# Kernel tuning notes

Measured on AMD Instinct MI355X. Metric: run time of the kernel, lower is better.

The kernel has to match this reference:

```python
import jax, jax.numpy as jnp
import numpy as np

B = 65536
IN2 = 256      # input_shape * 2
H2 = 512       # rnn_hidden_dim * 2
A = 32         # n_actions


def setup_inputs() -> dict:
    key = jax.random.key(0)
    ks = jax.random.split(key, 12)
    s = lambda k, shape, fan: jax.random.normal(k, shape, jnp.float32) / np.sqrt(fan)
    return {
        "inputs": jax.random.normal(ks[0], (B, IN2), jnp.float32),
        "hidden_state": jax.random.normal(ks[1], (B, H2), jnp.float32),
        "W1": s(ks[2], (H2, IN2), IN2),
        "b1": jnp.zeros((H2,), jnp.float32),
        "W_ih": s(ks[3], (3 * H2, H2), H2),
        "W_hh": s(ks[4], (3 * H2, H2), H2),
        "b_ih": jnp.zeros((3 * H2,), jnp.float32),
        "b_hh": jnp.zeros((3 * H2,), jnp.float32),
        "W21": s(ks[5], (A, H2), H2),
        "b21": jnp.zeros((A,), jnp.float32),
        "W22": s(ks[6], (A, H2), H2),
        "b22": jnp.zeros((A,), jnp.float32),
    }


def _forward(inputs, hidden_state, W1, b1, W_ih, W_hh, b_ih, b_hh, W21, b21, W22, b22):
    # fc1 + ReLU
    x = jax.nn.relu(inputs @ W1.T + b1)                      # [B, H2]
    h_in = hidden_state.reshape(-1, H2)
    # PyTorch GRUCell semantics
    gi = x @ W_ih.T + b_ih                                   # [B, 3*H2]
    gh = h_in @ W_hh.T + b_hh                                # [B, 3*H2]
    i_r, i_z, i_n = jnp.split(gi, 3, axis=1)
    h_r, h_z, h_n = jnp.split(gh, 3, axis=1)
    r = jax.nn.sigmoid(i_r + h_r)
    z = jax.nn.sigmoid(i_z + h_z)
    n = jnp.tanh(i_n + r * h_n)
    h = (1.0 - z) * n + z * h_in                             # [B, H2]
    # two Q heads
    q1 = h @ W21.T + b21                                     # [B, A]
    q2 = h @ W22.T + b22                                     # [B, A]
    # vectorized row-interleave (replaces the nested Python loop)
    q = jnp.stack([q1, q2], axis=1).reshape(2 * q1.shape[0], q1.shape[1])  # [2B, A]
    return q, h


def reference(inputs, hidden_state, W1, b1, W_ih, W_hh, b_ih, b_hh, W21, b21, W22, b22):
    return _forward(inputs, hidden_state, W1, b1, W_ih, W_hh, b_ih, b_hh, W21, b21, W22, b22)
```

## Files before the change

### kernel.cpp

```cpp
#include <hip/hip_runtime.h>


#define BATCH 65536
#define IN2   256
#define H2    512
#define NA    32
#define QELEMS (2 * BATCH * NA)

typedef float  f32x4  __attribute__((ext_vector_type(4)));
typedef short  short8 __attribute__((ext_vector_type(8)));
typedef __bf16 bf16x8 __attribute__((ext_vector_type(8)));

__device__ __forceinline__ f32x4 mfma16(short8 a, short8 b, f32x4 c) {
  return __builtin_amdgcn_mfma_f32_16x16x32_bf16(
      __builtin_bit_cast(bf16x8, a), __builtin_bit_cast(bf16x8, b), c, 0, 0, 0);
}

__device__ __forceinline__ unsigned short f2bf(float f) {
  union { float f; unsigned u; } v; v.f = f;
  unsigned r = v.u + 0x7fffu + ((v.u >> 16) & 1u);
  return (unsigned short)(r >> 16);
}

__global__ void cvt_kernel(const float* __restrict__ s,
                           unsigned short* __restrict__ d, int n4) {
  for (int i = blockIdx.x * blockDim.x + threadIdx.x; i < n4;
       i += gridDim.x * blockDim.x) {
    float4 f = ((const float4*)s)[i];
    ushort4 o;
    o.x = f2bf(f.x); o.y = f2bf(f.y); o.z = f2bf(f.z); o.w = f2bf(f.w);
    ((ushort4*)d)[i] = o;
  }
}

__global__ __launch_bounds__(256, 2)
void fc1_kernel(const unsigned short* __restrict__ A,
                const unsigned short* __restrict__ W,
                const float* __restrict__ bias,
                unsigned short* __restrict__ X) {
  __shared__ unsigned short As[128][72];
  __shared__ unsigned short Bs[64][72];
  const int tid  = threadIdx.x;
  const int lane = tid & 63, wid = tid >> 6;
  const int l16 = lane & 15, kg = (lane >> 4) * 8, rbase = (lane >> 4) * 4;
  const int row0 = blockIdx.x * 128;
  const int col0 = blockIdx.y * 64;
  const int wrow = (wid >> 1) * 64;
  const int wcol = (wid & 1) * 32;

  f32x4 acc[4][2] = {};

  for (int k0 = 0; k0 < IN2; k0 += 64) {
#pragma unroll
    for (int c = 0; c < 4; ++c) {
      int idx = tid + c * 256;
      int r = idx >> 3, k8 = idx & 7;
      uint4 v = *(const uint4*)&A[(row0 + r) * IN2 + k0 + k8 * 8];
      *(uint4*)&As[r][k8 * 8] = v;
    }
#pragma unroll
    for (int c = 0; c < 2; ++c) {
      int idx = tid + c * 256;
      int r = idx >> 3, k8 = idx & 7;
      uint4 v = *(const uint4*)&W[(col0 + r) * IN2 + k0 + k8 * 8];
      *(uint4*)&Bs[r][k8 * 8] = v;
    }
    __syncthreads();
#pragma unroll
    for (int kk = 0; kk < 64; kk += 32) {
      short8 af[4], bf[2];
#pragma unroll
      for (int m = 0; m < 4; ++m)
        af[m] = *(const short8*)&As[wrow + m * 16 + l16][kk + kg];
#pragma unroll
      for (int n = 0; n < 2; ++n)
        bf[n] = *(const short8*)&Bs[wcol + n * 16 + l16][kk + kg];
#pragma unroll
      for (int m = 0; m < 4; ++m)
#pragma unroll
        for (int n = 0; n < 2; ++n)
          acc[m][n] = mfma16(af[m], bf[n], acc[m][n]);
    }
    __syncthreads();
  }

#pragma unroll
  for (int m = 0; m < 4; ++m)
#pragma unroll
    for (int n = 0; n < 2; ++n) {
      int col = col0 + wcol + n * 16 + l16;
      float bv = bias[col];
#pragma unroll
      for (int e = 0; e < 4; ++e) {
        int row = row0 + wrow + m * 16 + rbase + e;
        float v = acc[m][n][e] + bv;
        v = v > 0.f ? v : 0.f;
        X[row * H2 + col] = f2bf(v);
      }
    }
}

__global__ __launch_bounds__(256, 2)
void gru_kernel(const unsigned short* __restrict__ X16,
                const unsigned short* __restrict__ H16,
                const unsigned short* __restrict__ Wih,
                const unsigned short* __restrict__ Whh,
                const float* __restrict__ b_ih,
                const float* __restrict__ b_hh,
                const float* __restrict__ hidden,
                float* __restrict__ out_h) {
  __shared__ unsigned short Xs[128][72];
  __shared__ unsigned short Hs[128][72];
  __shared__ unsigned short Ws[6][32][72];

  const int tid  = threadIdx.x;
  const int lane = tid & 63, wid = tid >> 6;
  const int l16 = lane & 15, kg = (lane >> 4) * 8, rbase = (lane >> 4) * 4;
  const int row0 = blockIdx.x * 128;
  const int j0   = blockIdx.y * 32;
  const int wrow = wid * 32;

  f32x4 accI[3][2][2] = {};
  f32x4 accH[3][2][2] = {};

  for (int k0 = 0; k0 < H2; k0 += 64) {
#pragma unroll
    for (int c = 0; c < 4; ++c) {
      int idx = tid + c * 256;
      int r = idx >> 3, k8 = idx & 7;
      *(uint4*)&Xs[r][k8 * 8] =
          *(const uint4*)&X16[(row0 + r) * H2 + k0 + k8 * 8];
    }
#pragma unroll
    for (int c = 0; c < 4; ++c) {
      int idx = tid + c * 256;
      int r = idx >> 3, k8 = idx & 7;
      *(uint4*)&Hs[r][k8 * 8] =
          *(const uint4*)&H16[(row0 + r) * H2 + k0 + k8 * 8];
    }
#pragma unroll
    for (int c = 0; c < 6; ++c) {
      int idx = tid + c * 256;
      int slab = idx >> 8, rem = idx & 255;
      int r = rem >> 3, k8 = rem & 7;
      const unsigned short* src =
          (slab < 3) ? &Wih[(slab * H2 + j0 + r) * H2]
                     : &Whh[((slab - 3) * H2 + j0 + r) * H2];
      *(uint4*)&Ws[slab][r][k8 * 8] = *(const uint4*)&src[k0 + k8 * 8];
    }
    __syncthreads();
#pragma unroll
    for (int kk = 0; kk < 64; kk += 32) {
      short8 ax[2], ah[2], bw[6][2];
#pragma unroll
      for (int m = 0; m < 2; ++m) {
        ax[m] = *(const short8*)&Xs[wrow + m * 16 + l16][kk + kg];
        ah[m] = *(const short8*)&Hs[wrow + m * 16 + l16][kk + kg];
      }
#pragma unroll
      for (int g = 0; g < 6; ++g)
#pragma unroll
        for (int n = 0; n < 2; ++n)
          bw[g][n] = *(const short8*)&Ws[g][n * 16 + l16][kk + kg];
#pragma unroll
      for (int g = 0; g < 3; ++g)
#pragma unroll
        for (int m = 0; m < 2; ++m)
#pragma unroll
          for (int n = 0; n < 2; ++n) {
            accI[g][m][n] = mfma16(ax[m], bw[g][n], accI[g][m][n]);
            accH[g][m][n] = mfma16(ah[m], bw[3 + g][n], accH[g][m][n]);
          }
    }
    __syncthreads();
  }

#pragma unroll
  for (int m = 0; m < 2; ++m)
#pragma unroll
    for (int n = 0; n < 2; ++n) {
      int j = j0 + n * 16 + l16;
      float bir = b_ih[j],        bhr = b_hh[j];
      float biz = b_ih[H2 + j],   bhz = b_hh[H2 + j];
      float bin = b_ih[2*H2 + j], bhn = b_hh[2*H2 + j];
#pragma unroll
      for (int e = 0; e < 4; ++e) {
        int row = row0 + wrow + m * 16 + rbase + e;
        float ir = accI[0][m][n][e] + bir;
        float iz = accI[1][m][n][e] + biz;
        float in_ = accI[2][m][n][e] + bin;
        float hr = accH[0][m][n][e] + bhr;
        float hz = accH[1][m][n][e] + bhz;
        float hn = accH[2][m][n][e] + bhn;
        float r = 1.f / (1.f + __expf(-(ir + hr)));
        float z = 1.f / (1.f + __expf(-(iz + hz)));
        float nn = tanhf(in_ + r * hn);
        float hp = hidden[row * H2 + j];
        out_h[row * H2 + j] = (1.f - z) * nn + z * hp;
      }
    }
}

__global__ __launch_bounds__(256, 2)
void heads_kernel(const float* __restrict__ Hsrc,
                  const unsigned short* __restrict__ Wq1,
                  const unsigned short* __restrict__ Wq2,
                  const float* __restrict__ b21,
                  const float* __restrict__ b22,
                  float* __restrict__ outq) {
  __shared__ unsigned short Hs[64][72];
  __shared__ unsigned short Wq[2][32][72];
  const int tid  = threadIdx.x;
  const int lane = tid & 63, wid = tid >> 6;
  const int l16 = lane & 15, kg = (lane >> 4) * 8, rbase = (lane >> 4) * 4;
  const int row0 = blockIdx.x * 64;
  const int wrow = wid * 16;

  f32x4 acc[2][2] = {};

  for (int k0 = 0; k0 < H2; k0 += 64) {
#pragma unroll
    for (int c = 0; c < 4; ++c) {
      int idx = tid + c * 256;
      int r = idx >> 4, c4 = idx & 15;
      float4 f = *(const float4*)&Hsrc[(row0 + r) * H2 + k0 + c4 * 4];
      ushort4 o;
      o.x = f2bf(f.x); o.y = f2bf(f.y); o.z = f2bf(f.z); o.w = f2bf(f.w);
      *(ushort4*)&Hs[r][c4 * 4] = o;
    }
#pragma unroll
    for (int c = 0; c < 2; ++c) {
      int idx = tid + c * 256;
      int slab = idx >> 8, rem = idx & 255;
      int r = rem >> 3, k8 = rem & 7;
      const unsigned short* src = slab ? Wq2 : Wq1;
      *(uint4*)&Wq[slab][r][k8 * 8] = *(const uint4*)&src[r * H2 + k0 + k8 * 8];
    }
    __syncthreads();
#pragma unroll
    for (int kk = 0; kk < 64; kk += 32) {
      short8 a = *(const short8*)&Hs[wrow + l16][kk + kg];
#pragma unroll
      for (int hd = 0; hd < 2; ++hd)
#pragma unroll
        for (int n = 0; n < 2; ++n) {
          short8 b = *(const short8*)&Wq[hd][n * 16 + l16][kk + kg];
          acc[hd][n] = mfma16(a, b, acc[hd][n]);
        }
    }
    __syncthreads();
  }

#pragma unroll
  for (int hd = 0; hd < 2; ++hd)
#pragma unroll
    for (int n = 0; n < 2; ++n) {
      int col = n * 16 + l16;
      float bv = hd ? b22[col] : b21[col];
#pragma unroll
      for (int e = 0; e < 4; ++e) {
        int row = row0 + wrow + rbase + e;
        outq[(2 * row + hd) * NA + col] = acc[hd][n][e] + bv;
      }
    }
}

extern "C" void kernel_launch(void* const* d_in, const int* in_sizes, int n_in,
                              void* d_out, int out_size, void* d_ws,
                              size_t ws_size, hipStream_t stream) {
  (void)in_sizes; (void)n_in; (void)out_size; (void)ws_size;
  const float* inputs = (const float*)d_in[0];
  const float* hidden = (const float*)d_in[1];
  const float* W1     = (const float*)d_in[2];
  const float* b1     = (const float*)d_in[3];
  const float* W_ih   = (const float*)d_in[4];
  const float* W_hh   = (const float*)d_in[5];
  const float* b_ih   = (const float*)d_in[6];
  const float* b_hh   = (const float*)d_in[7];
  const float* W21    = (const float*)d_in[8];
  const float* b21    = (const float*)d_in[9];
  const float* W22    = (const float*)d_in[10];
  const float* b22    = (const float*)d_in[11];
  float* out = (float*)d_out;

  char* ws = (char*)d_ws;
  size_t off = 0;
  unsigned short* in16  = (unsigned short*)(ws + off); off += (size_t)BATCH * IN2 * 2;
  unsigned short* h16   = (unsigned short*)(ws + off); off += (size_t)BATCH * H2 * 2;
  unsigned short* x16   = (unsigned short*)(ws + off); off += (size_t)BATCH * H2 * 2;
  unsigned short* W1_16 = (unsigned short*)(ws + off); off += (size_t)H2 * IN2 * 2;
  unsigned short* Wih16 = (unsigned short*)(ws + off); off += (size_t)3 * H2 * H2 * 2;
  unsigned short* Whh16 = (unsigned short*)(ws + off); off += (size_t)3 * H2 * H2 * 2;
  unsigned short* W2116 = (unsigned short*)(ws + off); off += (size_t)NA * H2 * 2;
  unsigned short* W2216 = (unsigned short*)(ws + off); off += (size_t)NA * H2 * 2;

  auto cvt = [&](const float* s, unsigned short* d, int n) {
    int n4 = n / 4;
    int blocks = (n4 + 255) / 256;
    if (blocks > 8192) blocks = 8192;
    cvt_kernel<<<blocks, 256, 0, stream>>>(s, d, n4);
  };
  cvt(inputs, in16, BATCH * IN2);
  cvt(hidden, h16, BATCH * H2);
  cvt(W1, W1_16, H2 * IN2);
  cvt(W_ih, Wih16, 3 * H2 * H2);
  cvt(W_hh, Whh16, 3 * H2 * H2);
  cvt(W21, W2116, NA * H2);
  cvt(W22, W2216, NA * H2);

  fc1_kernel<<<dim3(BATCH / 128, H2 / 64), 256, 0, stream>>>(in16, W1_16, b1, x16);

  float* out_h = out + QELEMS;
  gru_kernel<<<dim3(BATCH / 128, H2 / 32), 256, 0, stream>>>(
      x16, h16, Wih16, Whh16, b_ih, b_hh, hidden, out_h);

  heads_kernel<<<BATCH / 64, 256, 0, stream>>>(out_h, W2116, W2216, b21, b22, out);
}
```

Before: 791.2 us.

## Fuse input conversion into fc1, retile GRU with direct LDS loads, bf16 heads path

Drops the separate fp32-to-bf16 pass over the inputs by converting them inside fc1, and merges the weight conversions into one launch. The GRU kernel is retiled to 64 output columns per block with a swizzled LDS layout filled by global_load_lds. It folds the r/z gate GEMMs into shared accumulators, reads the previous hidden state from the bf16 copy, and uses a fast exp-based tanh. It optionally writes a bf16 copy of h so the heads kernel reads half the bytes. The cost is an extra bf16 store, and the previous-hidden blend and tanh now run at slightly lower precision.

New measurement: 644.2 us. 1.23x faster.

```diff
diff --git a/kernel.cpp b/kernel.cpp
--- a/kernel.cpp
+++ b/kernel.cpp
@@ -20,6 +20,24 @@
   union { float f; unsigned u; } v; v.f = f;
   unsigned r = v.u + 0x7fffu + ((v.u >> 16) & 1u);
   return (unsigned short)(r >> 16);
+}
+__device__ __forceinline__ float bf2f(unsigned short u) {
+  union { unsigned u; float f; } v; v.u = ((unsigned)u) << 16; return v.f;
+}
+
+__device__ __forceinline__ void gload16(const void* g, void* l) {
+  __builtin_amdgcn_global_load_lds(
+      (const __attribute__((address_space(1))) void*)g,
+      (__attribute__((address_space(3))) void*)l, 16, 0, 0);
+}
+
+__device__ __forceinline__ float sigm(float x) {
+  return 1.f / (1.f + __expf(-x));
+}
+__device__ __forceinline__ float tanh_fast(float x) {
+  float t = __expf(-2.f * fabsf(x));
+  float r = (1.f - t) / (1.f + t);
+  return x >= 0.f ? r : -r;
 }
 
 __global__ void cvt_kernel(const float* __restrict__ s,
@@ -33,8 +51,32 @@
   }
 }
 
+__global__ void cvtw_kernel(const float* __restrict__ W1,
+                            const float* __restrict__ Wih,
+                            const float* __restrict__ Whh,
+                            const float* __restrict__ W21,
+                            const float* __restrict__ W22,
+                            unsigned short* __restrict__ dW1,
+                            unsigned short* __restrict__ dWih,
+                            unsigned short* __restrict__ dWhh,
+                            unsigned short* __restrict__ dW21,
+                            unsigned short* __restrict__ dW22) {
+  int i = blockIdx.x * blockDim.x + threadIdx.x;
+  const float* s; unsigned short* d; int local;
+  if      (i < 32768)  { s = W1;  d = dW1;  local = i; }
+  else if (i < 229376) { s = Wih; d = dWih; local = i - 32768; }
+  else if (i < 425984) { s = Whh; d = dWhh; local = i - 229376; }
+  else if (i < 430080) { s = W21; d = dW21; local = i - 425984; }
+  else if (i < 434176) { s = W22; d = dW22; local = i - 430080; }
+  else return;
+  float4 f = ((const float4*)s)[local];
+  ushort4 o;
+  o.x = f2bf(f.x); o.y = f2bf(f.y); o.z = f2bf(f.z); o.w = f2bf(f.w);
+  ((ushort4*)d)[local] = o;
+}
+
 __global__ __launch_bounds__(256, 2)
-void fc1_kernel(const unsigned short* __restrict__ A,
+void fc1_kernel(const float* __restrict__ A,
                 const unsigned short* __restrict__ W,
                 const float* __restrict__ bias,
                 unsigned short* __restrict__ X) {
@@ -55,15 +97,22 @@
     for (int c = 0; c < 4; ++c) {
       int idx = tid + c * 256;
       int r = idx >> 3, k8 = idx & 7;
-      uint4 v = *(const uint4*)&A[(row0 + r) * IN2 + k0 + k8 * 8];
-      *(uint4*)&As[r][k8 * 8] = v;
+      const float* src = &A[(size_t)(row0 + r) * IN2 + k0 + k8 * 8];
+      float4 f0 = *(const float4*)src;
+      float4 f1 = *(const float4*)(src + 4);
+      uint4 o;
+      o.x = f2bf(f0.x) | ((unsigned)f2bf(f0.y) << 16);
+      o.y = f2bf(f0.z) | ((unsigned)f2bf(f0.w) << 16);
+      o.z = f2bf(f1.x) | ((unsigned)f2bf(f1.y) << 16);
+      o.w = f2bf(f1.z) | ((unsigned)f2bf(f1.w) << 16);
+      *(uint4*)&As[r][k8 * 8] = o;
     }
 #pragma unroll
     for (int c = 0; c < 2; ++c) {
       int idx = tid + c * 256;
       int r = idx >> 3, k8 = idx & 7;
-      uint4 v = *(const uint4*)&W[(col0 + r) * IN2 + k0 + k8 * 8];
-      *(uint4*)&Bs[r][k8 * 8] = v;
+      *(uint4*)&Bs[r][k8 * 8] =
+          *(const uint4*)&W[(size_t)(col0 + r) * IN2 + k0 + k8 * 8];
     }
     __syncthreads();
 #pragma unroll
@@ -95,7 +144,7 @@
         int row = row0 + wrow + m * 16 + rbase + e;
         float v = acc[m][n][e] + bv;
         v = v > 0.f ? v : 0.f;
-        X[row * H2 + col] = f2bf(v);
+        X[(size_t)row * H2 + col] = f2bf(v);
       }
     }
 }
@@ -107,107 +156,117 @@
                 const unsigned short* __restrict__ Whh,
                 const float* __restrict__ b_ih,
                 const float* __restrict__ b_hh,
-                const float* __restrict__ hidden,
-                float* __restrict__ out_h) {
-  __shared__ unsigned short Xs[128][72];
-  __shared__ unsigned short Hs[128][72];
-  __shared__ unsigned short Ws[6][32][72];
+                float* __restrict__ out_h,
+                unsigned short* __restrict__ h16b) {
+  __shared__ unsigned short lds[40960];
+  char* ldsb = (char*)lds;
 
   const int tid  = threadIdx.x;
   const int lane = tid & 63, wid = tid >> 6;
-  const int l16 = lane & 15, kg = (lane >> 4) * 8, rbase = (lane >> 4) * 4;
+  const int l16 = lane & 15;
   const int row0 = blockIdx.x * 128;
-  const int j0   = blockIdx.y * 32;
-  const int wrow = wid * 32;
-
-  f32x4 accI[3][2][2] = {};
-  f32x4 accH[3][2][2] = {};
+  const int j0   = blockIdx.y * 64;
+  const int wrow = (wid >> 1) * 64;
+  const int wcol = (wid & 1) * 32;
+
+  const int lr   = lane >> 3;
+  const int scol = ((lane & 7) ^ (lr & 7)) * 8;
+  const unsigned short* gx = X16 + (size_t)(row0 + wid * 32 + lr) * H2 + scol;
+  const unsigned short* gh = H16 + (size_t)(row0 + wid * 32 + lr) * H2 + scol;
+
+  f32x4 accR[4][2] = {}, accZ[4][2] = {}, accIN[4][2] = {}, accHN[4][2] = {};
 
   for (int k0 = 0; k0 < H2; k0 += 64) {
 #pragma unroll
-    for (int c = 0; c < 4; ++c) {
-      int idx = tid + c * 256;
-      int r = idx >> 3, k8 = idx & 7;
-      *(uint4*)&Xs[r][k8 * 8] =
-          *(const uint4*)&X16[(row0 + r) * H2 + k0 + k8 * 8];
-    }
-#pragma unroll
-    for (int c = 0; c < 4; ++c) {
-      int idx = tid + c * 256;
-      int r = idx >> 3, k8 = idx & 7;
-      *(uint4*)&Hs[r][k8 * 8] =
-          *(const uint4*)&H16[(row0 + r) * H2 + k0 + k8 * 8];
-    }
-#pragma unroll
-    for (int c = 0; c < 6; ++c) {
-      int idx = tid + c * 256;
-      int slab = idx >> 8, rem = idx & 255;
-      int r = rem >> 3, k8 = rem & 7;
+    for (int i = 0; i < 4; ++i) {
+      gload16(gx + k0 + i * 8 * H2, ldsb + (wid * 4 + i) * 1024);
+      gload16(gh + k0 + i * 8 * H2, ldsb + 16384 + (wid * 4 + i) * 1024);
+    }
+#pragma unroll
+    for (int i = 0; i < 12; ++i) {
+      int g = wid * 12 + i;
+      int s = g >> 3;
+      int r = (g & 7) * 8 + lr;
       const unsigned short* src =
-          (slab < 3) ? &Wih[(slab * H2 + j0 + r) * H2]
-                     : &Whh[((slab - 3) * H2 + j0 + r) * H2];
-      *(uint4*)&Ws[slab][r][k8 * 8] = *(const uint4*)&src[k0 + k8 * 8];
-    }
-    __syncthreads();
+          (s < 3) ? Wih + (size_t)(s * H2 + j0 + r) * H2
+                  : Whh + (size_t)((s - 3) * H2 + j0 + r) * H2;
+      gload16(src + k0 + scol, ldsb + 32768 + g * 1024);
+    }
+    __syncthreads();
+
 #pragma unroll
     for (int kk = 0; kk < 64; kk += 32) {
-      short8 ax[2], ah[2], bw[6][2];
-#pragma unroll
-      for (int m = 0; m < 2; ++m) {
-        ax[m] = *(const short8*)&Xs[wrow + m * 16 + l16][kk + kg];
-        ah[m] = *(const short8*)&Hs[wrow + m * 16 + l16][kk + kg];
-      }
-#pragma unroll
-      for (int g = 0; g < 6; ++g)
-#pragma unroll
-        for (int n = 0; n < 2; ++n)
-          bw[g][n] = *(const short8*)&Ws[g][n * 16 + l16][kk + kg];
-#pragma unroll
-      for (int g = 0; g < 3; ++g)
-#pragma unroll
-        for (int m = 0; m < 2; ++m)
-#pragma unroll
-          for (int n = 0; n < 2; ++n) {
-            accI[g][m][n] = mfma16(ax[m], bw[g][n], accI[g][m][n]);
-            accH[g][m][n] = mfma16(ah[m], bw[3 + g][n], accH[g][m][n]);
-          }
-    }
-    __syncthreads();
-  }
-
-#pragma unroll
-  for (int m = 0; m < 2; ++m)
-#pragma unroll
-    for (int n = 0; n < 2; ++n) {
-      int j = j0 + n * 16 + l16;
-      float bir = b_ih[j],        bhr = b_hh[j];
-      float biz = b_ih[H2 + j],   bhz = b_hh[H2 + j];
-      float bin = b_ih[2*H2 + j], bhn = b_hh[2*H2 + j];
+      const int cch = (kk >> 3) + (lane >> 4);
+      short8 ax[4], ah[4];
+#pragma unroll
+      for (int m = 0; m < 4; ++m) {
+        int r = wrow + m * 16 + l16;
+        int off = r * 128 + ((cch ^ (r & 7)) << 4);
+        ax[m] = *(const short8*)(ldsb + off);
+        ah[m] = *(const short8*)(ldsb + 16384 + off);
+      }
+#pragma unroll
+      for (int n = 0; n < 2; ++n) {
+        int rr = wcol + n * 16 + l16;
+        int woff = 32768 + rr * 128 + ((cch ^ (rr & 7)) << 4);
+        short8 b0 = *(const short8*)(ldsb + woff);
+        short8 b3 = *(const short8*)(ldsb + woff + 3 * 8192);
+#pragma unroll
+        for (int m = 0; m < 4; ++m) {
+          accR[m][n] = mfma16(ax[m], b0, accR[m][n]);
+          accR[m][n] = mfma16(ah[m], b3, accR[m][n]);
+        }
+        short8 b1 = *(const short8*)(ldsb + woff + 1 * 8192);
+        short8 b4 = *(const short8*)(ldsb + woff + 4 * 8192);
+#pragma unroll
+        for (int m = 0; m < 4; ++m) {
+          accZ[m][n] = mfma16(ax[m], b1, accZ[m][n]);
+          accZ[m][n] = mfma16(ah[m], b4, accZ[m][n]);
+        }
+        short8 b2 = *(const short8*)(ldsb + woff + 2 * 8192);
+        short8 b5 = *(const short8*)(ldsb + woff + 5 * 8192);
+#pragma unroll
+        for (int m = 0; m < 4; ++m) {
+          accIN[m][n] = mfma16(ax[m], b2, accIN[m][n]);
+          accHN[m][n] = mfma16(ah[m], b5, accHN[m][n]);
+        }
+      }
+    }
+    __syncthreads();
+  }
+
+  const int rbase = (lane >> 4) * 4;
+#pragma unroll
+  for (int n = 0; n < 2; ++n) {
+    int j = j0 + wcol + n * 16 + l16;
+    float brr = b_ih[j] + b_hh[j];
+    float bzz = b_ih[H2 + j] + b_hh[H2 + j];
+    float bin = b_ih[2 * H2 + j];
+    float bhn = b_hh[2 * H2 + j];
+#pragma unroll
+    for (int m = 0; m < 4; ++m) {
 #pragma unroll
       for (int e = 0; e < 4; ++e) {
         int row = row0 + wrow + m * 16 + rbase + e;
-        float ir = accI[0][m][n][e] + bir;
-        float iz = accI[1][m][n][e] + biz;
-        float in_ = accI[2][m][n][e] + bin;
-        float hr = accH[0][m][n][e] + bhr;
-        float hz = accH[1][m][n][e] + bhz;
-        float hn = accH[2][m][n][e] + bhn;
-        float r = 1.f / (1.f + __expf(-(ir + hr)));
-        float z = 1.f / (1.f + __expf(-(iz + hz)));
-        float nn = tanhf(in_ + r * hn);
-        float hp = hidden[row * H2 + j];
-        out_h[row * H2 + j] = (1.f - z) * nn + z * hp;
-      }
-    }
+        float r  = sigm(accR[m][n][e] + brr);
+        float z  = sigm(accZ[m][n][e] + bzz);
+        float nn = tanh_fast(accIN[m][n][e] + bin + r * (accHN[m][n][e] + bhn));
+        float hp = bf2f(H16[(size_t)row * H2 + j]);
+        float h  = (1.f - z) * nn + z * hp;
+        out_h[(size_t)row * H2 + j] = h;
+        if (h16b) h16b[(size_t)row * H2 + j] = f2bf(h);
+      }
+    }
+  }
 }
 
 __global__ __launch_bounds__(256, 2)
-void heads_kernel(const float* __restrict__ Hsrc,
-                  const unsigned short* __restrict__ Wq1,
-                  const unsigned short* __restrict__ Wq2,
-                  const float* __restrict__ b21,
-                  const float* __restrict__ b22,
-                  float* __restrict__ outq) {
+void heads_bf16_kernel(const unsigned short* __restrict__ Hsrc,
+                       const unsigned short* __restrict__ Wq1,
+                       const unsigned short* __restrict__ Wq2,
+                       const float* __restrict__ b21,
+                       const float* __restrict__ b22,
+                       float* __restrict__ outq) {
   __shared__ unsigned short Hs[64][72];
   __shared__ unsigned short Wq[2][32][72];
   const int tid  = threadIdx.x;
@@ -220,13 +279,11 @@
 
   for (int k0 = 0; k0 < H2; k0 += 64) {
 #pragma unroll
-    for (int c = 0; c < 4; ++c) {
-      int idx = tid + c * 256;
-      int r = idx >> 4, c4 = idx & 15;
-      float4 f = *(const float4*)&Hsrc[(row0 + r) * H2 + k0 + c4 * 4];
-      ushort4 o;
-      o.x = f2bf(f.x); o.y = f2bf(f.y); o.z = f2bf(f.z); o.w = f2bf(f.w);
-      *(ushort4*)&Hs[r][c4 * 4] = o;
+    for (int c = 0; c < 2; ++c) {
+      int idx = tid + c * 256;
+      int r = idx >> 3, k8 = idx & 7;
+      *(uint4*)&Hs[r][k8 * 8] =
+          *(const uint4*)&Hsrc[(size_t)(row0 + r) * H2 + k0 + k8 * 8];
     }
 #pragma unroll
     for (int c = 0; c < 2; ++c) {
@@ -234,7 +291,8 @@
       int slab = idx >> 8, rem = idx & 255;
       int r = rem >> 3, k8 = rem & 7;
       const unsigned short* src = slab ? Wq2 : Wq1;
-      *(uint4*)&Wq[slab][r][k8 * 8] = *(const uint4*)&src[r * H2 + k0 + k8 * 8];
+      *(uint4*)&Wq[slab][r][k8 * 8] =
+          *(const uint4*)&src[(size_t)r * H2 + k0 + k8 * 8];
     }
     __syncthreads();
 #pragma unroll
@@ -260,7 +318,72 @@
 #pragma unroll
       for (int e = 0; e < 4; ++e) {
         int row = row0 + wrow + rbase + e;
-        outq[(2 * row + hd) * NA + col] = acc[hd][n][e] + bv;
+        outq[(size_t)(2 * row + hd) * NA + col] = acc[hd][n][e] + bv;
+      }
+    }
+}
+
+__global__ __launch_bounds__(256, 2)
+void heads_f32_kernel(const float* __restrict__ Hsrc,
+                      const unsigned short* __restrict__ Wq1,
+                      const unsigned short* __restrict__ Wq2,
+                      const float* __restrict__ b21,
+                      const float* __restrict__ b22,
+                      float* __restrict__ outq) {
+  __shared__ unsigned short Hs[64][72];
+  __shared__ unsigned short Wq[2][32][72];
+  const int tid  = threadIdx.x;
+  const int lane = tid & 63, wid = tid >> 6;
+  const int l16 = lane & 15, kg = (lane >> 4) * 8, rbase = (lane >> 4) * 4;
+  const int row0 = blockIdx.x * 64;
+  const int wrow = wid * 16;
+
+  f32x4 acc[2][2] = {};
+
+  for (int k0 = 0; k0 < H2; k0 += 64) {
+#pragma unroll
+    for (int c = 0; c < 4; ++c) {
+      int idx = tid + c * 256;
+      int r = idx >> 4, c4 = idx & 15;
+      float4 f = *(const float4*)&Hsrc[(size_t)(row0 + r) * H2 + k0 + c4 * 4];
+      ushort4 o;
+      o.x = f2bf(f.x); o.y = f2bf(f.y); o.z = f2bf(f.z); o.w = f2bf(f.w);
+      *(ushort4*)&Hs[r][c4 * 4] = o;
+    }
+#pragma unroll
+    for (int c = 0; c < 2; ++c) {
+      int idx = tid + c * 256;
+      int slab = idx >> 8, rem = idx & 255;
+      int r = rem >> 3, k8 = rem & 7;
+      const unsigned short* src = slab ? Wq2 : Wq1;
+      *(uint4*)&Wq[slab][r][k8 * 8] =
+          *(const uint4*)&src[(size_t)r * H2 + k0 + k8 * 8];
+    }
+    __syncthreads();
+#pragma unroll
+    for (int kk = 0; kk < 64; kk += 32) {
+      short8 a = *(const short8*)&Hs[wrow + l16][kk + kg];
+#pragma unroll
+      for (int hd = 0; hd < 2; ++hd)
+#pragma unroll
+        for (int n = 0; n < 2; ++n) {
+          short8 b = *(const short8*)&Wq[hd][n * 16 + l16][kk + kg];
+          acc[hd][n] = mfma16(a, b, acc[hd][n]);
+        }
+    }
+    __syncthreads();
+  }
+
+#pragma unroll
+  for (int hd = 0; hd < 2; ++hd)
+#pragma unroll
+    for (int n = 0; n < 2; ++n) {
+      int col = n * 16 + l16;
+      float bv = hd ? b22[col] : b21[col];
+#pragma unroll
+      for (int e = 0; e < 4; ++e) {
+        int row = row0 + wrow + rbase + e;
+        outq[(size_t)(2 * row + hd) * NA + col] = acc[hd][n][e] + bv;
       }
     }
 }
@@ -268,7 +391,7 @@
 extern "C" void kernel_launch(void* const* d_in, const int* in_sizes, int n_in,
                               void* d_out, int out_size, void* d_ws,
                               size_t ws_size, hipStream_t stream) {
-  (void)in_sizes; (void)n_in; (void)out_size; (void)ws_size;
+  (void)in_sizes; (void)n_in; (void)out_size;
   const float* inputs = (const float*)d_in[0];
   const float* hidden = (const float*)d_in[1];
   const float* W1     = (const float*)d_in[2];
@@ -285,7 +408,6 @@
 
   char* ws = (char*)d_ws;
   size_t off = 0;
-  unsigned short* in16  = (unsigned short*)(ws + off); off += (size_t)BATCH * IN2 * 2;
   unsigned short* h16   = (unsigned short*)(ws + off); off += (size_t)BATCH * H2 * 2;
   unsigned short* x16   = (unsigned short*)(ws + off); off += (size_t)BATCH * H2 * 2;
   unsigned short* W1_16 = (unsigned short*)(ws + off); off += (size_t)H2 * IN2 * 2;
@@ -293,26 +415,23 @@
   unsigned short* Whh16 = (unsigned short*)(ws + off); off += (size_t)3 * H2 * H2 * 2;
   unsigned short* W2116 = (unsigned short*)(ws + off); off += (size_t)NA * H2 * 2;
   unsigned short* W2216 = (unsigned short*)(ws + off); off += (size_t)NA * H2 * 2;
-
-  auto cvt = [&](const float* s, unsigned short* d, int n) {
-    int n4 = n / 4;
-    int blocks = (n4 + 255) / 256;
-    if (blocks > 8192) blocks = 8192;
-    cvt_kernel<<<blocks, 256, 0, stream>>>(s, d, n4);
-  };
-  cvt(inputs, in16, BATCH * IN2);
-  cvt(hidden, h16, BATCH * H2);
-  cvt(W1, W1_16, H2 * IN2);
-  cvt(W_ih, Wih16, 3 * H2 * H2);
-  cvt(W_hh, Whh16, 3 * H2 * H2);
-  cvt(W21, W2116, NA * H2);
-  cvt(W22, W2216, NA * H2);
-
-  fc1_kernel<<<dim3(BATCH / 128, H2 / 64), 256, 0, stream>>>(in16, W1_16, b1, x16);
+  size_t base_need = off;
+  unsigned short* h16b = nullptr;
+  if (ws_size >= base_need + (size_t)BATCH * H2 * 2)
+    h16b = (unsigned short*)(ws + base_need);
+
+  cvt_kernel<<<8192, 256, 0, stream>>>(hidden, h16, BATCH * H2 / 4);
+  cvtw_kernel<<<1696, 256, 0, stream>>>(W1, W_ih, W_hh, W21, W22,
+                                        W1_16, Wih16, Whh16, W2116, W2216);
+
+  fc1_kernel<<<dim3(BATCH / 128, H2 / 64), 256, 0, stream>>>(inputs, W1_16, b1, x16);
 
   float* out_h = out + QELEMS;
-  gru_kernel<<<dim3(BATCH / 128, H2 / 32), 256, 0, stream>>>(
-      x16, h16, Wih16, Whh16, b_ih, b_hh, hidden, out_h);
-
-  heads_kernel<<<BATCH / 64, 256, 0, stream>>>(out_h, W2116, W2216, b21, b22, out);
-}
+  gru_kernel<<<dim3(BATCH / 128, H2 / 64), 256, 0, stream>>>(
+      x16, h16, Wih16, Whh16, b_ih, b_hh, out_h, h16b);
+
+  if (h16b)
+    heads_bf16_kernel<<<BATCH / 64, 256, 0, stream>>>(h16b, W2116, W2216, b21, b22, out);
+  else
+    heads_f32_kernel<<<BATCH / 64, 256, 0, stream>>>(out_h, W2116, W2216, b21, b22, out);
+}
```
